# Performance work log

Hardware: AMD Instinct MI355X
Metric: run time of the kernel (lower is better)

The kernel has to match this reference:

```python
import jax, jax.numpy as jnp
import numpy as np

E = 32          # n_routed_experts / num_local_experts
H = 1024        # hidden_size
I = 512         # moe_intermediate_size
G = 8           # n_group
TKG = 4         # topk_group
TOPK = 8        # num_experts_per_tok
NSH = 2         # n_shared_experts
SCALE = 2.5     # routed_scaling_factor


def setup_inputs() -> dict:
    key = jax.random.key(0)
    ks = jax.random.split(key, 10)
    s = 0.02
    return {
        "hidden_states": jax.random.normal(ks[0], (2, 1024, H), jnp.float32),
        # router: linear weight [E, H] and e_score_correction_bias [E]
        "gate_w": jax.random.normal(ks[1], (E, H), jnp.float32) * s,
        "gate_bias": jax.random.normal(ks[2], (E,), jnp.float32) * s,
        # routed experts (stacked SwiGLU weights, torch Linear layout [out, in])
        "w_gate": jax.random.normal(ks[3], (E, I, H), jnp.float32) * s,
        "w_up": jax.random.normal(ks[4], (E, I, H), jnp.float32) * s,
        "w_down": jax.random.normal(ks[5], (E, H, I), jnp.float32) * s,
        # shared experts: one MLP with intermediate = I * NSH
        "sh_gate": jax.random.normal(ks[6], (I * NSH, H), jnp.float32) * s,
        "sh_up": jax.random.normal(ks[7], (I * NSH, H), jnp.float32) * s,
        "sh_down": jax.random.normal(ks[8], (H, I * NSH), jnp.float32) * s,
    }


def reference(hidden_states, gate_w, gate_bias, w_gate, w_up, w_down,
              sh_gate, sh_up, sh_down):
    B, S, Hd = hidden_states.shape
    h = hidden_states.reshape(-1, Hd)                      # [T, H]

    # ---- router (DeepseekV3TopkRouter + route_tokens_to_experts) ----
    logits = h.astype(jnp.float32) @ gate_w.T              # [T, E]
    scores = jax.nn.sigmoid(logits)
    sc = scores + gate_bias                                # scores_for_choice
    # group score = sum of top-2 expert scores within each group
    grp = sc.reshape(-1, G, E // G)                        # [T, G, E/G]
    group_scores = jax.lax.top_k(grp, 2)[0].sum(-1)        # [T, G]
    gidx = jax.lax.top_k(group_scores, TKG)[1]             # [T, TKG]
    gmask = jnp.sum(jax.nn.one_hot(gidx, G, dtype=sc.dtype), axis=1)  # [T, G]
    smask = jnp.repeat(gmask, E // G, axis=1)              # [T, E]
    masked = jnp.where(smask > 0, sc, jnp.zeros_like(sc))  # masked_fill(~mask, 0)
    tki = jax.lax.top_k(masked, TOPK)[1]                   # [T, TOPK]
    tkw = jnp.take_along_axis(scores, tki, axis=1)         # gather raw sigmoid scores
    tkw = tkw / (tkw.sum(-1, keepdims=True) + 1e-20)       # norm_topk_prob
    tkw = tkw * SCALE

    # ---- dispatch-compute-combine (experts_forward) ----
    # combine[t, e] = sum_k tkw[t, k] * [tki[t, k] == e]
    combine = (jax.nn.one_hot(tki, E, dtype=tkw.dtype) * tkw[..., None]).sum(1)  # [T, E]
    g = jax.nn.silu(jnp.einsum('th,eih->tei', h, w_gate))  # [T, E, I]
    u = jnp.einsum('th,eih->tei', h, w_up)                 # [T, E, I]
    routed = jnp.einsum('tei,ehi->th', g * u * combine[:, :, None], w_down)  # [T, H]

    # ---- shared experts ----
    sg = jax.nn.silu(h @ sh_gate.T)
    shared = (sg * (h @ sh_up.T)) @ sh_down.T              # [T, H]

    return (routed + shared).reshape(B, S, Hd)
```

## Files before the change

kernel.cpp:

```cpp
#include <hip/hip_runtime.h>
#include <hip/hip_bf16.h>
#include <cstdint>

#define E_ 32
#define H_ 1024
#define I_ 512
#define G_ 8
#define NSH_ 2
#define SCALE_ 2.5f
#define NROUTED (E_ * I_)
#define PADCAP (16384 + E_ * 128)

typedef unsigned short u16;
using bf16x8_t = __attribute__((ext_vector_type(8))) __bf16;
using f32x4_t  = __attribute__((ext_vector_type(4))) float;

__device__ __forceinline__ u16 f2bf(float x) {
  union { float f; uint32_t u; } v; v.f = x;
  uint32_t u = v.u;
  uint32_t r = (u + 0x7fffu + ((u >> 16) & 1u)) >> 16;
  return (u16)r;
}
__device__ __forceinline__ float bf2f(u16 x) {
  union { uint32_t u; float f; } v; v.u = ((uint32_t)x) << 16; return v.f;
}

__device__ __forceinline__ void load_lds16(const void* g, void* l) {
  __builtin_amdgcn_global_load_lds(
      (const __attribute__((address_space(1))) unsigned int*)g,
      (__attribute__((address_space(3))) unsigned int*)l,
      16, 0, 0);
}

__global__ void cvt_kernel(const float* __restrict__ src, u16* __restrict__ dst, long n4) {
  long i = (long)blockIdx.x * blockDim.x + threadIdx.x;
  if (i >= n4) return;
  float4 v = ((const float4*)src)[i];
  ushort4 o;
  o.x = f2bf(v.x); o.y = f2bf(v.y); o.z = f2bf(v.z); o.w = f2bf(v.w);
  ((ushort4*)dst)[i] = o;
}

#define W4_WG  4194304L
#define W4_WU  8388608L
#define W4_WD  12582912L
#define W4_SHG 12845056L
#define W4_SHU 13107200L
#define W4_TOT 13369344L
__global__ void cvtw_kernel(const float* __restrict__ wg, const float* __restrict__ wu,
                            const float* __restrict__ wd, const float* __restrict__ shg,
                            const float* __restrict__ shu, const float* __restrict__ shd,
                            u16* __restrict__ dst) {
  long i = (long)blockIdx.x * blockDim.x + threadIdx.x;
  long stride = (long)gridDim.x * blockDim.x;
  for (; i < W4_TOT; i += stride) {
    const float* s; long off;
    if (i < W4_WG)       { s = wg;  off = i; }
    else if (i < W4_WU)  { s = wu;  off = i - W4_WG; }
    else if (i < W4_WD)  { s = wd;  off = i - W4_WU; }
    else if (i < W4_SHG) { s = shg; off = i - W4_WD; }
    else if (i < W4_SHU) { s = shu; off = i - W4_SHG; }
    else                 { s = shd; off = i - W4_SHU; }
    float4 v = ((const float4*)s)[off];
    ushort4 o;
    o.x = f2bf(v.x); o.y = f2bf(v.y); o.z = f2bf(v.z); o.w = f2bf(v.w);
    ((ushort4*)dst)[i] = o;
  }
}

__global__ void init_kernel(int* __restrict__ counts, int* __restrict__ cursor,
                            int* __restrict__ tok_list, float* __restrict__ wt_list) {
  int i = blockIdx.x * blockDim.x + threadIdx.x;
  if (i < PADCAP) { tok_list[i] = 0; wt_list[i] = 0.f; }
  if (i < E_) { counts[i] = 0; cursor[i] = 0; }
}

__global__ void gwt_kernel(const float* __restrict__ gw, float* __restrict__ gwT) {
  int i = blockIdx.x * blockDim.x + threadIdx.x;
  if (i >= H_ * E_) return;
  int k = i >> 5, e = i & 31;
  gwT[i] = gw[(long)e * H_ + k];
}

__global__ __launch_bounds__(256) void logits_kernel(
    const float* __restrict__ h, const float* __restrict__ gwT,
    float* __restrict__ logits) {
  __shared__ float sh[8][H_];
  const int tid = threadIdx.x;
  const int t0 = blockIdx.x * 8;
  #pragma unroll
  for (int c = tid; c < 8 * H_ / 4; c += 256) {
    int row = c / (H_ / 4), col = c % (H_ / 4);
    ((float4*)sh[row])[col] = ((const float4*)(h + (size_t)(t0 + row) * H_))[col];
  }
  __syncthreads();
  const int w = tid >> 6, l = tid & 63;
  const int e = l & 31, tl = w * 2 + (l >> 5);
  const float* hp = sh[tl];
  const float* wp = gwT + e;
  float acc = 0.f;
  #pragma unroll 8
  for (int k = 0; k < H_; ++k) acc += hp[k] * wp[(size_t)k * E_];
  logits[(size_t)(t0 + tl) * E_ + e] = acc;
}

__global__ __launch_bounds__(256) void topk_kernel(
    const float* __restrict__ logits, const float* __restrict__ gb,
    int* __restrict__ idx8, float* __restrict__ wt8, int* __restrict__ counts) {
  __shared__ float s_sc[256][33];
  const int lt = threadIdx.x;
  const int t = blockIdx.x * 256 + lt;
  float sc[E_];
  #pragma unroll
  for (int e = 0; e < E_; ++e) {
    float lg = logits[(size_t)t * E_ + e];
    float sig = 1.f / (1.f + __expf(-lg));
    s_sc[lt][e] = sig;
    sc[e] = sig + gb[e];
  }
  float gs[G_];
  #pragma unroll
  for (int g = 0; g < G_; ++g) {
    float a = sc[g * 4], b = sc[g * 4 + 1], c = sc[g * 4 + 2], d = sc[g * 4 + 3];
    float hi1 = fmaxf(a, b), lo1 = fminf(a, b);
    float hi2 = fmaxf(c, d), lo2 = fminf(c, d);
    float m1 = fmaxf(hi1, hi2);
    float m2 = (hi1 >= hi2) ? fmaxf(lo1, hi2) : fmaxf(lo2, hi1);
    gs[g] = m1 + m2;
  }
  unsigned gm = 0;
  #pragma unroll
  for (int r = 0; r < 4; ++r) {
    float bv = -1e30f; int bi = 0;
    #pragma unroll
    for (int g = 0; g < G_; ++g)
      if (!(gm & (1u << g)) && gs[g] > bv) { bv = gs[g]; bi = g; }
    gm |= 1u << bi;
  }
  float msk[E_];
  #pragma unroll
  for (int e = 0; e < E_; ++e)
    msk[e] = ((gm >> (e >> 2)) & 1u) ? sc[e] : 0.f;
  unsigned um = 0; float wsum = 0.f;
  int idxs[8]; float wts[8];
  #pragma unroll
  for (int r = 0; r < 8; ++r) {
    float bv = -1e30f; int bi = 0;
    #pragma unroll
    for (int e = 0; e < E_; ++e)
      if (!(um & (1u << e)) && msk[e] > bv) { bv = msk[e]; bi = e; }
    um |= 1u << bi;
    idxs[r] = bi;
    float wv = s_sc[lt][bi];
    wts[r] = wv; wsum += wv;
  }
  float inv = SCALE_ / (wsum + 1e-20f);
  #pragma unroll
  for (int r = 0; r < 8; ++r) {
    idx8[(size_t)t * 8 + r] = idxs[r];
    wt8[(size_t)t * 8 + r] = wts[r] * inv;
    atomicAdd(&counts[idxs[r]], 1);
  }
}

__global__ void scan_kernel(const int* __restrict__ counts, int* __restrict__ offs) {
  if (threadIdx.x == 0 && blockIdx.x == 0) {
    int run = 0;
    for (int e = 0; e < E_; ++e) {
      offs[e] = run;
      run += ((counts[e] + 127) >> 7) << 7;
    }
    offs[E_] = run;
  }
}

__global__ void fill_kernel(const int* __restrict__ idx8, const float* __restrict__ wt8,
                            const int* __restrict__ offs, int* __restrict__ cursor,
                            int* __restrict__ tok_list, float* __restrict__ wt_list,
                            int* __restrict__ pair_pos, int npair) {
  int i = blockIdx.x * blockDim.x + threadIdx.x;
  if (i >= npair) return;
  int e = idx8[i];
  int p = atomicAdd(&cursor[e], 1);
  int slot = offs[e] + p;
  tok_list[slot] = i >> 3;
  wt_list[slot] = wt8[i];
  pair_pos[i] = slot;
}

__global__ __launch_bounds__(256, 4) void p1_kernel(
    const u16* __restrict__ hbf,
    const u16* __restrict__ bg, const u16* __restrict__ bu,
    const u16* __restrict__ bshg, const u16* __restrict__ bshu,
    const int* __restrict__ counts, const int* __restrict__ offs,
    const int* __restrict__ tok_list, const float* __restrict__ wt_list,
    u16* __restrict__ gu,
    u16* __restrict__ gu_sh,
    int T) {
  const int z = blockIdx.z, tt = blockIdx.y, nb = blockIdx.x;
  const bool sh_e = (z == E_);
  if (!sh_e && nb >= 8) return;
  const int cnt = sh_e ? T : counts[z];
  if (tt * 128 >= cnt) return;
  const int off = sh_e ? 0 : offs[z];

  __shared__ u16 lsA[128 * 64];
  __shared__ u16 lsB0[64 * 64];
  __shared__ u16 lsB1[64 * 64];
  __shared__ int s_tok[128];
  __shared__ float s_wt[128];

  const int tid = threadIdx.x;
  if (tid < 128) {
    if (sh_e) { s_tok[tid] = tt * 128 + tid; s_wt[tid] = 1.0f; }
    else {
      int slot = off + tt * 128 + tid;
      s_tok[tid] = tok_list[slot];
      s_wt[tid] = wt_list[slot];
    }
  }
  __syncthreads();

  const u16* Bg = sh_e ? (bshg + (size_t)(nb * 64) * H_)
                       : (bg + ((size_t)z * I_ + nb * 64) * H_);
  const u16* Bu = sh_e ? (bshu + (size_t)(nb * 64) * H_)
                       : (bu + ((size_t)z * I_ + nb * 64) * H_);

  const int w = tid >> 6, l = tid & 63;
  const int wr = w >> 1, wc = w & 1;
  const int lr = l & 15, lh = l >> 4;
  const int sw = lr & 7;

  f32x4_t acc0[4][2], acc1[4][2];
  #pragma unroll
  for (int m = 0; m < 4; ++m)
    #pragma unroll
    for (int n = 0; n < 2; ++n) {
      acc0[m][n] = (f32x4_t){0.f, 0.f, 0.f, 0.f};
      acc1[m][n] = (f32x4_t){0.f, 0.f, 0.f, 0.f};
    }

  for (int k0 = 0; k0 < H_; k0 += 64) {
    #pragma unroll
    for (int i = 0; i < 4; ++i) {
      int c = tid + 256 * i;
      int row = c >> 3, cb = c & 7;
      int scb = cb ^ (row & 7);
      load_lds16(hbf + (size_t)s_tok[row] * H_ + k0 + scb * 8, (char*)lsA + c * 16);
    }
    #pragma unroll
    for (int i = 0; i < 2; ++i) {
      int c = tid + 256 * i;
      int row = c >> 3, cb = c & 7;
      int scb = cb ^ (row & 7);
      load_lds16(Bg + (size_t)row * H_ + k0 + scb * 8, (char*)lsB0 + c * 16);
      load_lds16(Bu + (size_t)row * H_ + k0 + scb * 8, (char*)lsB1 + c * 16);
    }
    __syncthreads();
    #pragma unroll
    for (int kk = 0; kk < 64; kk += 32) {
      const int sb = kk >> 3;
      const int blk = ((sb + lh) ^ sw) << 3;
      bf16x8_t af[4], b0f[2], b1f[2];
      #pragma unroll
      for (int m = 0; m < 4; ++m)
        af[m] = *(const bf16x8_t*)(lsA + (wr * 64 + m * 16 + lr) * 64 + blk);
      #pragma unroll
      for (int n = 0; n < 2; ++n) {
        b0f[n] = *(const bf16x8_t*)(lsB0 + (wc * 32 + n * 16 + lr) * 64 + blk);
        b1f[n] = *(const bf16x8_t*)(lsB1 + (wc * 32 + n * 16 + lr) * 64 + blk);
      }
      #pragma unroll
      for (int m = 0; m < 4; ++m)
        #pragma unroll
        for (int n = 0; n < 2; ++n) {
          acc0[m][n] = __builtin_amdgcn_mfma_f32_16x16x32_bf16(af[m], b0f[n], acc0[m][n], 0, 0, 0);
          acc1[m][n] = __builtin_amdgcn_mfma_f32_16x16x32_bf16(af[m], b1f[n], acc1[m][n], 0, 0, 0);
        }
    }
    __syncthreads();
  }

  const int ldo = sh_e ? (I_ * NSH_) : I_;
  u16* outp = sh_e ? (gu_sh + (size_t)(tt * 128) * ldo + nb * 64)
                   : (gu + (size_t)(off + tt * 128) * ldo + nb * 64);
  #pragma unroll
  for (int m = 0; m < 4; ++m) {
    #pragma unroll
    for (int n = 0; n < 2; ++n) {
      int col = wc * 32 + n * 16 + lr;
      #pragma unroll
      for (int j = 0; j < 4; ++j) {
        int trow = wr * 64 + m * 16 + lh * 4 + j;
        float gv = acc0[m][n][j], uv = acc1[m][n][j];
        float sv = gv / (1.f + __expf(-gv));
        outp[(size_t)trow * ldo + col] = f2bf(sv * uv * s_wt[trow]);
      }
    }
  }
}

__global__ __launch_bounds__(256, 6) void p2_kernel(
    const u16* __restrict__ gu, const u16* __restrict__ gu_sh,
    const u16* __restrict__ bd,
    const u16* __restrict__ bshd,
    const int* __restrict__ counts, const int* __restrict__ offs,
    u16* __restrict__ part,
    u16* __restrict__ part_sh,
    int T) {
  const int z = blockIdx.z, tt = blockIdx.y, nb = blockIdx.x;
  const bool sh_e = (z == E_);
  const int cnt = sh_e ? T : counts[z];
  if (tt * 128 >= cnt) return;

  __shared__ u16 lsA[128 * 64];
  __shared__ u16 lsB[64 * 64];

  const int tid = threadIdx.x;
  const int w = tid >> 6, l = tid & 63;
  const int wr = w >> 1, wc = w & 1;
  const int lr = l & 15, lh = l >> 4;
  const int sw = lr & 7;

  const int K = sh_e ? (I_ * NSH_) : I_;
  const int NT = K / 64;
  const u16* Ab = sh_e ? (gu_sh + (size_t)(tt * 128) * K)
                       : (gu + (size_t)(offs[z] + tt * 128) * K);
  const u16* Bb = sh_e ? (bshd + (size_t)(nb * 64) * K)
                       : (bd + (size_t)z * H_ * I_ + (size_t)(nb * 64) * K);
  u16* outp = sh_e ? (part_sh + (size_t)(tt * 128) * H_ + nb * 64)
                   : (part + (size_t)(offs[z] + tt * 128) * H_ + nb * 64);

  f32x4_t acc[4][2];
  #pragma unroll
  for (int m = 0; m < 4; ++m)
    #pragma unroll
    for (int n = 0; n < 2; ++n) acc[m][n] = (f32x4_t){0.f, 0.f, 0.f, 0.f};

  for (int s = 0; s < NT; ++s) {
    int k0 = s * 64;
    #pragma unroll
    for (int i = 0; i < 4; ++i) {
      int c = tid + 256 * i;
      int row = c >> 3, cb = c & 7;
      int scb = cb ^ (row & 7);
      load_lds16(Ab + (size_t)row * K + k0 + scb * 8, (char*)lsA + c * 16);
    }
    #pragma unroll
    for (int i = 0; i < 2; ++i) {
      int c = tid + 256 * i;
      int row = c >> 3, cb = c & 7;
      int scb = cb ^ (row & 7);
      load_lds16(Bb + (size_t)row * K + k0 + scb * 8, (char*)lsB + c * 16);
    }
    __syncthreads();
    #pragma unroll
    for (int kk = 0; kk < 64; kk += 32) {
      const int sb = kk >> 3;
      const int blk = ((sb + lh) ^ sw) << 3;
      bf16x8_t af[4], bf[2];
      #pragma unroll
      for (int m = 0; m < 4; ++m)
        af[m] = *(const bf16x8_t*)(lsA + (wr * 64 + m * 16 + lr) * 64 + blk);
      #pragma unroll
      for (int n = 0; n < 2; ++n)
        bf[n] = *(const bf16x8_t*)(lsB + (wc * 32 + n * 16 + lr) * 64 + blk);
      #pragma unroll
      for (int m = 0; m < 4; ++m)
        #pragma unroll
        for (int n = 0; n < 2; ++n)
          acc[m][n] = __builtin_amdgcn_mfma_f32_16x16x32_bf16(af[m], bf[n], acc[m][n], 0, 0, 0);
    }
    __syncthreads();
  }

  #pragma unroll
  for (int m = 0; m < 4; ++m) {
    #pragma unroll
    for (int n = 0; n < 2; ++n) {
      int col = wc * 32 + n * 16 + lr;
      #pragma unroll
      for (int j = 0; j < 4; ++j) {
        int trow = wr * 64 + m * 16 + lh * 4 + j;
        outp[(size_t)trow * H_ + col] = f2bf(acc[m][n][j]);
      }
    }
  }
}

__global__ void combine_kernel(const u16* __restrict__ part, const u16* __restrict__ part_sh,
                               const int* __restrict__ pair_pos, float* __restrict__ out) {
  int t = blockIdx.x;
  int h = threadIdx.x * 4;
  int pp[8];
  #pragma unroll
  for (int s = 0; s < 8; ++s) pp[s] = pair_pos[(long)t * 8 + s];
  ushort4 v = *(const ushort4*)(part_sh + (size_t)t * H_ + h);
  float a0 = bf2f(v.x), a1 = bf2f(v.y), a2 = bf2f(v.z), a3 = bf2f(v.w);
  #pragma unroll
  for (int s = 0; s < 8; ++s) {
    ushort4 u = *(const ushort4*)(part + (size_t)pp[s] * H_ + h);
    a0 += bf2f(u.x); a1 += bf2f(u.y); a2 += bf2f(u.z); a3 += bf2f(u.w);
  }
  float4 o = {a0, a1, a2, a3};
  *(float4*)(out + (size_t)t * H_ + h) = o;
}

extern "C" void kernel_launch(void* const* d_in, const int* in_sizes, int n_in,
                              void* d_out, int out_size, void* d_ws, size_t ws_size,
                              hipStream_t stream) {
  const float* hs  = (const float*)d_in[0];
  const float* gw  = (const float*)d_in[1];
  const float* gb  = (const float*)d_in[2];
  const float* wg  = (const float*)d_in[3];
  const float* wu  = (const float*)d_in[4];
  const float* wd  = (const float*)d_in[5];
  const float* shg = (const float*)d_in[6];
  const float* shu = (const float*)d_in[7];
  const float* shd = (const float*)d_in[8];
  float* out = (float*)d_out;

  const int T = in_sizes[0] / H_;

  char* ws = (char*)d_ws;
  size_t off = 0;
  auto alloc = [&](size_t bytes) {
    char* p = ws + off;
    off += (bytes + 255) & ~(size_t)255;
    return p;
  };
  int*   counts   = (int*)alloc(E_ * 4);
  int*   cursor   = (int*)alloc(E_ * 4);
  int*   offsv    = (int*)alloc((E_ + 1) * 4);
  int*   idx8     = (int*)alloc((size_t)T * 8 * 4);
  float* wt8      = (float*)alloc((size_t)T * 8 * 4);
  int*   pair_pos = (int*)alloc((size_t)T * 8 * 4);
  int*   tok_list = (int*)alloc(PADCAP * 4);
  float* wt_list  = (float*)alloc(PADCAP * 4);
  float* gwT      = (float*)alloc((size_t)H_ * E_ * 4);
  float* logits   = (float*)alloc((size_t)T * E_ * 4);
  u16* hbf     = (u16*)alloc((size_t)T * H_ * 2);
  u16* wbf     = (u16*)alloc((size_t)W4_TOT * 4 * 2);
  u16* gu      = (u16*)alloc((size_t)PADCAP * I_ * 2);
  u16* gu_sh   = (u16*)alloc((size_t)T * I_ * NSH_ * 2);
  u16* part    = (u16*)alloc((size_t)PADCAP * H_ * 2);
  u16* part_sh = (u16*)alloc((size_t)T * H_ * 2);
  if (off > ws_size) return;

  u16* bg   = wbf;
  u16* bu   = wbf + (size_t)NROUTED * H_;
  u16* bd   = bu + (size_t)NROUTED * H_;
  u16* bshg = bd + (size_t)E_ * H_ * I_;
  u16* bshu = bshg + (size_t)I_ * NSH_ * H_;
  u16* bshd = bshu + (size_t)I_ * NSH_ * H_;

  hipLaunchKernelGGL(init_kernel, dim3((PADCAP + 255) / 256), dim3(256), 0, stream,
                     counts, cursor, tok_list, wt_list);

  hipLaunchKernelGGL(gwt_kernel, dim3((H_ * E_ + 255) / 256), dim3(256), 0, stream, gw, gwT);
  hipLaunchKernelGGL(logits_kernel, dim3(T / 8), dim3(256), 0, stream, hs, gwT, logits);
  hipLaunchKernelGGL(topk_kernel, dim3(T / 256), dim3(256), 0, stream,
                     logits, gb, idx8, wt8, counts);
  hipLaunchKernelGGL(scan_kernel, dim3(1), dim3(64), 0, stream, counts, offsv);
  hipLaunchKernelGGL(fill_kernel, dim3((T * 8 + 255) / 256), dim3(256), 0, stream,
                     idx8, wt8, offsv, cursor, tok_list, wt_list, pair_pos, T * 8);

  {
    long n4 = (long)T * H_ / 4;
    hipLaunchKernelGGL(cvt_kernel, dim3((int)((n4 + 255) / 256)), dim3(256), 0, stream,
                       hs, hbf, n4);
  }
  hipLaunchKernelGGL(cvtw_kernel, dim3(2048), dim3(256), 0, stream,
                     wg, wu, wd, shg, shu, shd, wbf);

  hipLaunchKernelGGL(p1_kernel, dim3(16, T / 128, E_ + 1), dim3(256), 0, stream,
                     hbf, bg, bu, bshg, bshu, counts, offsv, tok_list, wt_list,
                     gu, gu_sh, T);

  hipLaunchKernelGGL(p2_kernel, dim3(16, T / 128, E_ + 1), dim3(256), 0, stream,
                     gu, gu_sh, bd, bshd, counts, offsv, part, part_sh, T);

  hipLaunchKernelGGL(combine_kernel, dim3(T), dim3(256), 0, stream,
                     part, part_sh, pair_pos, out);
}
```

Before: 312.4 us.

## Persistent atomic tile queues for expert GEMMs and fuse small prep kernels

```diff
diff --git a/kernel.cpp b/kernel.cpp
--- a/kernel.cpp
+++ b/kernel.cpp
@@ -32,66 +32,59 @@
       16, 0, 0);
 }
 
-__global__ void cvt_kernel(const float* __restrict__ src, u16* __restrict__ dst, long n4) {
-  long i = (long)blockIdx.x * blockDim.x + threadIdx.x;
-  if (i >= n4) return;
-  float4 v = ((const float4*)src)[i];
-  ushort4 o;
-  o.x = f2bf(v.x); o.y = f2bf(v.y); o.z = f2bf(v.z); o.w = f2bf(v.w);
-  ((ushort4*)dst)[i] = o;
-}
-
-#define W4_WG  4194304L
-#define W4_WU  8388608L
-#define W4_WD  12582912L
-#define W4_SHG 12845056L
-#define W4_SHU 13107200L
-#define W4_TOT 13369344L
+#define OFF_BU   16777216L
+#define OFF_BD   33554432L
+#define OFF_BSHG 50331648L
+#define OFF_BSHU 51380224L
+#define OFF_BSHD 52428800L
+#define WBF_TOT  53477376L
+
+__global__ void init_kernel(const float* __restrict__ gw, float* __restrict__ gwT,
+                            int* __restrict__ counts, int* __restrict__ cursor,
+                            int* __restrict__ qheads,
+                            int* __restrict__ tok_list, float* __restrict__ wt_list) {
+  int i = blockIdx.x * blockDim.x + threadIdx.x;
+  if (i < H_ * E_) {
+    int k = i >> 5, e = i & 31;
+    gwT[i] = gw[(long)e * H_ + k];
+  }
+  if (i < PADCAP) { tok_list[i] = 0; wt_list[i] = 0.f; }
+  if (i < E_) { counts[i] = 0; cursor[i] = 0; }
+  if (i < 2) qheads[i] = 0;
+}
+
 __global__ void cvtw_kernel(const float* __restrict__ wg, const float* __restrict__ wu,
-                            const float* __restrict__ wd, const float* __restrict__ shg,
-                            const float* __restrict__ shu, const float* __restrict__ shd,
-                            u16* __restrict__ dst) {
+                            const float* __restrict__ shg, const float* __restrict__ shu,
+                            u16* __restrict__ wbf) {
   long i = (long)blockIdx.x * blockDim.x + threadIdx.x;
   long stride = (long)gridDim.x * blockDim.x;
-  for (; i < W4_TOT; i += stride) {
-    const float* s; long off;
-    if (i < W4_WG)       { s = wg;  off = i; }
-    else if (i < W4_WU)  { s = wu;  off = i - W4_WG; }
-    else if (i < W4_WD)  { s = wd;  off = i - W4_WU; }
-    else if (i < W4_SHG) { s = shg; off = i - W4_WD; }
-    else if (i < W4_SHU) { s = shu; off = i - W4_SHG; }
-    else                 { s = shd; off = i - W4_SHU; }
+  for (; i < 8912896L; i += stride) {
+    const float* s; long off; long dofs;
+    if (i < 4194304L)      { s = wg;  off = i;            dofs = i * 4; }
+    else if (i < 8388608L) { s = wu;  off = i - 4194304L; dofs = OFF_BU + off * 4; }
+    else if (i < 8650752L) { s = shg; off = i - 8388608L; dofs = OFF_BSHG + off * 4; }
+    else                   { s = shu; off = i - 8650752L; dofs = OFF_BSHU + off * 4; }
     float4 v = ((const float4*)s)[off];
     ushort4 o;
     o.x = f2bf(v.x); o.y = f2bf(v.y); o.z = f2bf(v.z); o.w = f2bf(v.w);
-    ((ushort4*)dst)[i] = o;
-  }
-}
-
-__global__ void init_kernel(int* __restrict__ counts, int* __restrict__ cursor,
-                            int* __restrict__ tok_list, float* __restrict__ wt_list) {
-  int i = blockIdx.x * blockDim.x + threadIdx.x;
-  if (i < PADCAP) { tok_list[i] = 0; wt_list[i] = 0.f; }
-  if (i < E_) { counts[i] = 0; cursor[i] = 0; }
-}
-
-__global__ void gwt_kernel(const float* __restrict__ gw, float* __restrict__ gwT) {
-  int i = blockIdx.x * blockDim.x + threadIdx.x;
-  if (i >= H_ * E_) return;
-  int k = i >> 5, e = i & 31;
-  gwT[i] = gw[(long)e * H_ + k];
+    *(ushort4*)(wbf + dofs) = o;
+  }
 }
 
 __global__ __launch_bounds__(256) void logits_kernel(
     const float* __restrict__ h, const float* __restrict__ gwT,
-    float* __restrict__ logits) {
+    float* __restrict__ logits, u16* __restrict__ hbf) {
   __shared__ float sh[8][H_];
   const int tid = threadIdx.x;
   const int t0 = blockIdx.x * 8;
   #pragma unroll
   for (int c = tid; c < 8 * H_ / 4; c += 256) {
     int row = c / (H_ / 4), col = c % (H_ / 4);
-    ((float4*)sh[row])[col] = ((const float4*)(h + (size_t)(t0 + row) * H_))[col];
+    float4 v = ((const float4*)(h + (size_t)(t0 + row) * H_))[col];
+    ((float4*)sh[row])[col] = v;
+    ushort4 o;
+    o.x = f2bf(v.x); o.y = f2bf(v.y); o.z = f2bf(v.z); o.w = f2bf(v.w);
+    ((ushort4*)(hbf + (size_t)(t0 + row) * H_))[col] = o;
   }
   __syncthreads();
   const int w = tid >> 6, l = tid & 63;
@@ -163,26 +156,20 @@
   }
 }
 
-__global__ void scan_kernel(const int* __restrict__ counts, int* __restrict__ offs) {
-  if (threadIdx.x == 0 && blockIdx.x == 0) {
-    int run = 0;
-    for (int e = 0; e < E_; ++e) {
-      offs[e] = run;
-      run += ((counts[e] + 127) >> 7) << 7;
-    }
-    offs[E_] = run;
-  }
-}
-
 __global__ void fill_kernel(const int* __restrict__ idx8, const float* __restrict__ wt8,
-                            const int* __restrict__ offs, int* __restrict__ cursor,
+                            const int* __restrict__ counts, int* __restrict__ cursor,
                             int* __restrict__ tok_list, float* __restrict__ wt_list,
                             int* __restrict__ pair_pos, int npair) {
   int i = blockIdx.x * blockDim.x + threadIdx.x;
   if (i >= npair) return;
   int e = idx8[i];
+  int offz = 0;
+  for (int k = 0; k < E_; ++k) {
+    if (k == e) break;
+    offz += ((counts[k] + 127) >> 7) << 7;
+  }
   int p = atomicAdd(&cursor[e], 1);
-  int slot = offs[e] + p;
+  int slot = offz + p;
   tok_list[slot] = i >> 3;
   wt_list[slot] = wt8[i];
   pair_pos[i] = slot;
@@ -190,199 +177,260 @@
 
 __global__ __launch_bounds__(256, 4) void p1_kernel(
     const u16* __restrict__ hbf,
-    const u16* __restrict__ bg, const u16* __restrict__ bu,
-    const u16* __restrict__ bshg, const u16* __restrict__ bshu,
-    const int* __restrict__ counts, const int* __restrict__ offs,
+    const u16* __restrict__ wbf,
+    const int* __restrict__ counts,
     const int* __restrict__ tok_list, const float* __restrict__ wt_list,
+    int* __restrict__ qheads,
+    const float* __restrict__ wd, const float* __restrict__ shd,
+    u16* __restrict__ wbf_mut,
     u16* __restrict__ gu,
     u16* __restrict__ gu_sh,
     int T) {
-  const int z = blockIdx.z, tt = blockIdx.y, nb = blockIdx.x;
-  const bool sh_e = (z == E_);
-  if (!sh_e && nb >= 8) return;
-  const int cnt = sh_e ? T : counts[z];
-  if (tt * 128 >= cnt) return;
-  const int off = sh_e ? 0 : offs[z];
-
   __shared__ u16 lsA[128 * 64];
   __shared__ u16 lsB0[64 * 64];
   __shared__ u16 lsB1[64 * 64];
   __shared__ int s_tok[128];
   __shared__ float s_wt[128];
+  __shared__ int s_cnt[E_], s_off[E_], s_ntt[E_];
+  __shared__ int s_tot, s_tile;
 
   const int tid = threadIdx.x;
-  if (tid < 128) {
-    if (sh_e) { s_tok[tid] = tt * 128 + tid; s_wt[tid] = 1.0f; }
-    else {
-      int slot = off + tt * 128 + tid;
-      s_tok[tid] = tok_list[slot];
-      s_wt[tid] = wt_list[slot];
-    }
-  }
+  if (tid < E_) s_cnt[tid] = counts[tid];
   __syncthreads();
-
-  const u16* Bg = sh_e ? (bshg + (size_t)(nb * 64) * H_)
-                       : (bg + ((size_t)z * I_ + nb * 64) * H_);
-  const u16* Bu = sh_e ? (bshu + (size_t)(nb * 64) * H_)
-                       : (bu + ((size_t)z * I_ + nb * 64) * H_);
+  if (tid == 0) {
+    int run = 0, tot = 0;
+    for (int e = 0; e < E_; ++e) {
+      s_off[e] = run;
+      int nt = (s_cnt[e] + 127) >> 7;
+      s_ntt[e] = nt;
+      run += nt << 7;
+      tot += nt * 8;
+    }
+    s_tot = tot + (T / 128) * 16;
+  }
 
   const int w = tid >> 6, l = tid & 63;
   const int wr = w >> 1, wc = w & 1;
   const int lr = l & 15, lh = l >> 4;
   const int sw = lr & 7;
 
-  f32x4_t acc0[4][2], acc1[4][2];
-  #pragma unroll
-  for (int m = 0; m < 4; ++m)
+  for (;;) {
+    __syncthreads();
+    if (tid == 0) s_tile = atomicAdd(&qheads[0], 1);
+    __syncthreads();
+    int q = s_tile;
+    if (q >= s_tot) break;
+
+    int z = 0, rem = q;
+    for (; z < E_; ++z) { int t = s_ntt[z] * 8; if (rem < t) break; rem -= t; }
+    const bool sh_e = (z == E_);
+    int tt, nb;
+    if (sh_e) { tt = rem >> 4; nb = rem & 15; }
+    else      { tt = rem >> 3; nb = rem & 7; }
+    const int off = sh_e ? 0 : s_off[z];
+
+    if (tid < 128) {
+      if (sh_e) { s_tok[tid] = tt * 128 + tid; s_wt[tid] = 1.0f; }
+      else {
+        int slot = off + tt * 128 + tid;
+        s_tok[tid] = tok_list[slot];
+        s_wt[tid] = wt_list[slot];
+      }
+    }
+    __syncthreads();
+
+    const u16* Bg = sh_e ? (wbf + OFF_BSHG + (size_t)(nb * 64) * H_)
+                         : (wbf + ((size_t)z * I_ + nb * 64) * H_);
+    const u16* Bu = sh_e ? (wbf + OFF_BSHU + (size_t)(nb * 64) * H_)
+                         : (wbf + OFF_BU + ((size_t)z * I_ + nb * 64) * H_);
+
+    f32x4_t acc0[4][2], acc1[4][2];
     #pragma unroll
-    for (int n = 0; n < 2; ++n) {
-      acc0[m][n] = (f32x4_t){0.f, 0.f, 0.f, 0.f};
-      acc1[m][n] = (f32x4_t){0.f, 0.f, 0.f, 0.f};
-    }
-
-  for (int k0 = 0; k0 < H_; k0 += 64) {
+    for (int m = 0; m < 4; ++m)
+      #pragma unroll
+      for (int n = 0; n < 2; ++n) {
+        acc0[m][n] = (f32x4_t){0.f, 0.f, 0.f, 0.f};
+        acc1[m][n] = (f32x4_t){0.f, 0.f, 0.f, 0.f};
+      }
+
+    for (int k0 = 0; k0 < H_; k0 += 64) {
+      #pragma unroll
+      for (int i = 0; i < 4; ++i) {
+        int c = tid + 256 * i;
+        int row = c >> 3, cb = c & 7;
+        int scb = cb ^ (row & 7);
+        load_lds16(hbf + (size_t)s_tok[row] * H_ + k0 + scb * 8, (char*)lsA + c * 16);
+      }
+      #pragma unroll
+      for (int i = 0; i < 2; ++i) {
+        int c = tid + 256 * i;
+        int row = c >> 3, cb = c & 7;
+        int scb = cb ^ (row & 7);
+        load_lds16(Bg + (size_t)row * H_ + k0 + scb * 8, (char*)lsB0 + c * 16);
+        load_lds16(Bu + (size_t)row * H_ + k0 + scb * 8, (char*)lsB1 + c * 16);
+      }
+      __syncthreads();
+      #pragma unroll
+      for (int kk = 0; kk < 64; kk += 32) {
+        const int sb = kk >> 3;
+        const int blk = ((sb + lh) ^ sw) << 3;
+        bf16x8_t af[4], b0f[2], b1f[2];
+        #pragma unroll
+        for (int m = 0; m < 4; ++m)
+          af[m] = *(const bf16x8_t*)(lsA + (wr * 64 + m * 16 + lr) * 64 + blk);
+        #pragma unroll
+        for (int n = 0; n < 2; ++n) {
+          b0f[n] = *(const bf16x8_t*)(lsB0 + (wc * 32 + n * 16 + lr) * 64 + blk);
+          b1f[n] = *(const bf16x8_t*)(lsB1 + (wc * 32 + n * 16 + lr) * 64 + blk);
+        }
+        #pragma unroll
+        for (int m = 0; m < 4; ++m)
+          #pragma unroll
+          for (int n = 0; n < 2; ++n) {
+            acc0[m][n] = __builtin_amdgcn_mfma_f32_16x16x32_bf16(af[m], b0f[n], acc0[m][n], 0, 0, 0);
+            acc1[m][n] = __builtin_amdgcn_mfma_f32_16x16x32_bf16(af[m], b1f[n], acc1[m][n], 0, 0, 0);
+          }
+      }
+      __syncthreads();
+    }
+
+    const int ldo = sh_e ? (I_ * NSH_) : I_;
+    u16* outp = sh_e ? (gu_sh + (size_t)(tt * 128) * ldo + nb * 64)
+                     : (gu + (size_t)(off + tt * 128) * ldo + nb * 64);
     #pragma unroll
-    for (int i = 0; i < 4; ++i) {
-      int c = tid + 256 * i;
-      int row = c >> 3, cb = c & 7;
-      int scb = cb ^ (row & 7);
-      load_lds16(hbf + (size_t)s_tok[row] * H_ + k0 + scb * 8, (char*)lsA + c * 16);
-    }
-    #pragma unroll
-    for (int i = 0; i < 2; ++i) {
-      int c = tid + 256 * i;
-      int row = c >> 3, cb = c & 7;
-      int scb = cb ^ (row & 7);
-      load_lds16(Bg + (size_t)row * H_ + k0 + scb * 8, (char*)lsB0 + c * 16);
-      load_lds16(Bu + (size_t)row * H_ + k0 + scb * 8, (char*)lsB1 + c * 16);
-    }
-    __syncthreads();
-    #pragma unroll
-    for (int kk = 0; kk < 64; kk += 32) {
-      const int sb = kk >> 3;
-      const int blk = ((sb + lh) ^ sw) << 3;
-      bf16x8_t af[4], b0f[2], b1f[2];
-      #pragma unroll
-      for (int m = 0; m < 4; ++m)
-        af[m] = *(const bf16x8_t*)(lsA + (wr * 64 + m * 16 + lr) * 64 + blk);
+    for (int m = 0; m < 4; ++m) {
       #pragma unroll
       for (int n = 0; n < 2; ++n) {
-        b0f[n] = *(const bf16x8_t*)(lsB0 + (wc * 32 + n * 16 + lr) * 64 + blk);
-        b1f[n] = *(const bf16x8_t*)(lsB1 + (wc * 32 + n * 16 + lr) * 64 + blk);
-      }
-      #pragma unroll
-      for (int m = 0; m < 4; ++m)
-        #pragma unroll
-        for (int n = 0; n < 2; ++n) {
-          acc0[m][n] = __builtin_amdgcn_mfma_f32_16x16x32_bf16(af[m], b0f[n], acc0[m][n], 0, 0, 0);
-          acc1[m][n] = __builtin_amdgcn_mfma_f32_16x16x32_bf16(af[m], b1f[n], acc1[m][n], 0, 0, 0);
+        int col = wc * 32 + n * 16 + lr;
+        #pragma unroll
+        for (int j = 0; j < 4; ++j) {
+          int trow = wr * 64 + m * 16 + lh * 4 + j;
+          float gv = acc0[m][n][j], uv = acc1[m][n][j];
+          float sv = gv / (1.f + __expf(-gv));
+          outp[(size_t)trow * ldo + col] = f2bf(sv * uv * s_wt[trow]);
         }
-    }
-    __syncthreads();
-  }
-
-  const int ldo = sh_e ? (I_ * NSH_) : I_;
-  u16* outp = sh_e ? (gu_sh + (size_t)(tt * 128) * ldo + nb * 64)
-                   : (gu + (size_t)(off + tt * 128) * ldo + nb * 64);
-  #pragma unroll
-  for (int m = 0; m < 4; ++m) {
-    #pragma unroll
-    for (int n = 0; n < 2; ++n) {
-      int col = wc * 32 + n * 16 + lr;
-      #pragma unroll
-      for (int j = 0; j < 4; ++j) {
-        int trow = wr * 64 + m * 16 + lh * 4 + j;
-        float gv = acc0[m][n][j], uv = acc1[m][n][j];
-        float sv = gv / (1.f + __expf(-gv));
-        outp[(size_t)trow * ldo + col] = f2bf(sv * uv * s_wt[trow]);
-      }
-    }
+      }
+    }
+  }
+
+  const long WD4 = 4194304L, TOT4 = 4456448L;
+  for (long i = (long)blockIdx.x * 256 + tid; i < TOT4; i += (long)gridDim.x * 256) {
+    float4 v; long dofs;
+    if (i < WD4) { v = ((const float4*)wd)[i]; dofs = OFF_BD + i * 4; }
+    else { v = ((const float4*)shd)[i - WD4]; dofs = OFF_BSHD + (i - WD4) * 4; }
+    ushort4 o;
+    o.x = f2bf(v.x); o.y = f2bf(v.y); o.z = f2bf(v.z); o.w = f2bf(v.w);
+    *(ushort4*)(wbf_mut + dofs) = o;
   }
 }
 
 __global__ __launch_bounds__(256, 6) void p2_kernel(
     const u16* __restrict__ gu, const u16* __restrict__ gu_sh,
-    const u16* __restrict__ bd,
-    const u16* __restrict__ bshd,
-    const int* __restrict__ counts, const int* __restrict__ offs,
+    const u16* __restrict__ wbf,
+    const int* __restrict__ counts,
+    int* __restrict__ qheads,
     u16* __restrict__ part,
     u16* __restrict__ part_sh,
     int T) {
-  const int z = blockIdx.z, tt = blockIdx.y, nb = blockIdx.x;
-  const bool sh_e = (z == E_);
-  const int cnt = sh_e ? T : counts[z];
-  if (tt * 128 >= cnt) return;
-
   __shared__ u16 lsA[128 * 64];
   __shared__ u16 lsB[64 * 64];
+  __shared__ int s_cnt[E_], s_off[E_], s_ntt[E_];
+  __shared__ int s_tot, s_tile;
 
   const int tid = threadIdx.x;
+  if (tid < E_) s_cnt[tid] = counts[tid];
+  __syncthreads();
+  if (tid == 0) {
+    int run = 0, tot = 0;
+    for (int e = 0; e < E_; ++e) {
+      s_off[e] = run;
+      int nt = (s_cnt[e] + 127) >> 7;
+      s_ntt[e] = nt;
+      run += nt << 7;
+      tot += nt * 16;
+    }
+    s_tot = tot + (T / 128) * 16;
+  }
+
   const int w = tid >> 6, l = tid & 63;
   const int wr = w >> 1, wc = w & 1;
   const int lr = l & 15, lh = l >> 4;
   const int sw = lr & 7;
 
-  const int K = sh_e ? (I_ * NSH_) : I_;
-  const int NT = K / 64;
-  const u16* Ab = sh_e ? (gu_sh + (size_t)(tt * 128) * K)
-                       : (gu + (size_t)(offs[z] + tt * 128) * K);
-  const u16* Bb = sh_e ? (bshd + (size_t)(nb * 64) * K)
-                       : (bd + (size_t)z * H_ * I_ + (size_t)(nb * 64) * K);
-  u16* outp = sh_e ? (part_sh + (size_t)(tt * 128) * H_ + nb * 64)
-                   : (part + (size_t)(offs[z] + tt * 128) * H_ + nb * 64);
-
-  f32x4_t acc[4][2];
-  #pragma unroll
-  for (int m = 0; m < 4; ++m)
+  for (;;) {
+    __syncthreads();
+    if (tid == 0) s_tile = atomicAdd(&qheads[1], 1);
+    __syncthreads();
+    int q = s_tile;
+    if (q >= s_tot) break;
+
+    int z = 0, rem = q;
+    for (; z < E_; ++z) { int t = s_ntt[z] * 16; if (rem < t) break; rem -= t; }
+    const bool sh_e = (z == E_);
+    int tt = rem >> 4, nb = rem & 15;
+
+    const int K = sh_e ? (I_ * NSH_) : I_;
+    const int NT = K / 64;
+    const u16* Ab = sh_e ? (gu_sh + (size_t)(tt * 128) * K)
+                         : (gu + (size_t)(s_off[z] + tt * 128) * K);
+    const u16* Bb = sh_e ? (wbf + OFF_BSHD + (size_t)(nb * 64) * K)
+                         : (wbf + OFF_BD + (size_t)z * H_ * I_ + (size_t)(nb * 64) * K);
+    u16* outp = sh_e ? (part_sh + (size_t)(tt * 128) * H_ + nb * 64)
+                     : (part + (size_t)(s_off[z] + tt * 128) * H_ + nb * 64);
+
+    f32x4_t acc[4][2];
     #pragma unroll
-    for (int n = 0; n < 2; ++n) acc[m][n] = (f32x4_t){0.f, 0.f, 0.f, 0.f};
-
-  for (int s = 0; s < NT; ++s) {
-    int k0 = s * 64;
+    for (int m = 0; m < 4; ++m)
+      #pragma unroll
+      for (int n = 0; n < 2; ++n) acc[m][n] = (f32x4_t){0.f, 0.f, 0.f, 0.f};
+
+    for (int s = 0; s < NT; ++s) {
+      int k0 = s * 64;
+      #pragma unroll
+      for (int i = 0; i < 4; ++i) {
+        int c = tid + 256 * i;
+        int row = c >> 3, cb = c & 7;
+        int scb = cb ^ (row & 7);
+        load_lds16(Ab + (size_t)row * K + k0 + scb * 8, (char*)lsA + c * 16);
+      }
+      #pragma unroll
+      for (int i = 0; i < 2; ++i) {
+        int c = tid + 256 * i;
+        int row = c >> 3, cb = c & 7;
+        int scb = cb ^ (row & 7);
+        load_lds16(Bb + (size_t)row * K + k0 + scb * 8, (char*)lsB + c * 16);
+      }
+      __syncthreads();
+      #pragma unroll
+      for (int kk = 0; kk < 64; kk += 32) {
+        const int sb = kk >> 3;
+        const int blk = ((sb + lh) ^ sw) << 3;
+        bf16x8_t af[4], bf[2];
+        #pragma unroll
+        for (int m = 0; m < 4; ++m)
+          af[m] = *(const bf16x8_t*)(lsA + (wr * 64 + m * 16 + lr) * 64 + blk);
+        #pragma unroll
+        for (int n = 0; n < 2; ++n)
+          bf[n] = *(const bf16x8_t*)(lsB + (wc * 32 + n * 16 + lr) * 64 + blk);
+        #pragma unroll
+        for (int m = 0; m < 4; ++m)
+          #pragma unroll
+          for (int n = 0; n < 2; ++n)
+            acc[m][n] = __builtin_amdgcn_mfma_f32_16x16x32_bf16(af[m], bf[n], acc[m][n], 0, 0, 0);
+      }
+      __syncthreads();
+    }
+
     #pragma unroll
-    for (int i = 0; i < 4; ++i) {
-      int c = tid + 256 * i;
-      int row = c >> 3, cb = c & 7;
-      int scb = cb ^ (row & 7);
-      load_lds16(Ab + (size_t)row * K + k0 + scb * 8, (char*)lsA + c * 16);
-    }
-    #pragma unroll
-    for (int i = 0; i < 2; ++i) {
-      int c = tid + 256 * i;
-      int row = c >> 3, cb = c & 7;
-      int scb = cb ^ (row & 7);
-      load_lds16(Bb + (size_t)row * K + k0 + scb * 8, (char*)lsB + c * 16);
-    }
-    __syncthreads();
-    #pragma unroll
-    for (int kk = 0; kk < 64; kk += 32) {
-      const int sb = kk >> 3;
-      const int blk = ((sb + lh) ^ sw) << 3;
-      bf16x8_t af[4], bf[2];
-      #pragma unroll
-      for (int m = 0; m < 4; ++m)
-        af[m] = *(const bf16x8_t*)(lsA + (wr * 64 + m * 16 + lr) * 64 + blk);
-      #pragma unroll
-      for (int n = 0; n < 2; ++n)
-        bf[n] = *(const bf16x8_t*)(lsB + (wc * 32 + n * 16 + lr) * 64 + blk);
-      #pragma unroll
-      for (int m = 0; m < 4; ++m)
-        #pragma unroll
-        for (int n = 0; n < 2; ++n)
-          acc[m][n] = __builtin_amdgcn_mfma_f32_16x16x32_bf16(af[m], bf[n], acc[m][n], 0, 0, 0);
-    }
-    __syncthreads();
-  }
-
-  #pragma unroll
-  for (int m = 0; m < 4; ++m) {
-    #pragma unroll
-    for (int n = 0; n < 2; ++n) {
-      int col = wc * 32 + n * 16 + lr;
-      #pragma unroll
-      for (int j = 0; j < 4; ++j) {
-        int trow = wr * 64 + m * 16 + lh * 4 + j;
-        outp[(size_t)trow * H_ + col] = f2bf(acc[m][n][j]);
+    for (int m = 0; m < 4; ++m) {
+      #pragma unroll
+      for (int n = 0; n < 2; ++n) {
+        int col = wc * 32 + n * 16 + lr;
+        #pragma unroll
+        for (int j = 0; j < 4; ++j) {
+          int trow = wr * 64 + m * 16 + lh * 4 + j;
+          outp[(size_t)trow * H_ + col] = f2bf(acc[m][n][j]);
+        }
       }
     }
   }
@@ -431,7 +479,7 @@
   };
   int*   counts   = (int*)alloc(E_ * 4);
   int*   cursor   = (int*)alloc(E_ * 4);
-  int*   offsv    = (int*)alloc((E_ + 1) * 4);
+  int*   qheads   = (int*)alloc(2 * 4);
   int*   idx8     = (int*)alloc((size_t)T * 8 * 4);
   float* wt8      = (float*)alloc((size_t)T * 8 * 4);
   int*   pair_pos = (int*)alloc((size_t)T * 8 * 4);
@@ -440,45 +488,32 @@
   float* gwT      = (float*)alloc((size_t)H_ * E_ * 4);
   float* logits   = (float*)alloc((size_t)T * E_ * 4);
   u16* hbf     = (u16*)alloc((size_t)T * H_ * 2);
-  u16* wbf     = (u16*)alloc((size_t)W4_TOT * 4 * 2);
+  u16* wbf     = (u16*)alloc((size_t)WBF_TOT * 2);
   u16* gu      = (u16*)alloc((size_t)PADCAP * I_ * 2);
   u16* gu_sh   = (u16*)alloc((size_t)T * I_ * NSH_ * 2);
   u16* part    = (u16*)alloc((size_t)PADCAP * H_ * 2);
   u16* part_sh = (u16*)alloc((size_t)T * H_ * 2);
   if (off > ws_size) return;
 
-  u16* bg   = wbf;
-  u16* bu   = wbf + (size_t)NROUTED * H_;
-  u16* bd   = bu + (size_t)NROUTED * H_;
-  u16* bshg = bd + (size_t)E_ * H_ * I_;
-  u16* bshu = bshg + (size_t)I_ * NSH_ * H_;
-  u16* bshd = bshu + (size_t)I_ * NSH_ * H_;
-
-  hipLaunchKernelGGL(init_kernel, dim3((PADCAP + 255) / 256), dim3(256), 0, stream,
-                     counts, cursor, tok_list, wt_list);
-
-  hipLaunchKernelGGL(gwt_kernel, dim3((H_ * E_ + 255) / 256), dim3(256), 0, stream, gw, gwT);
-  hipLaunchKernelGGL(logits_kernel, dim3(T / 8), dim3(256), 0, stream, hs, gwT, logits);
+  hipLaunchKernelGGL(init_kernel, dim3(128), dim3(256), 0, stream,
+                     gw, gwT, counts, cursor, qheads, tok_list, wt_list);
+
+  hipLaunchKernelGGL(logits_kernel, dim3(T / 8), dim3(256), 0, stream,
+                     hs, gwT, logits, hbf);
   hipLaunchKernelGGL(topk_kernel, dim3(T / 256), dim3(256), 0, stream,
                      logits, gb, idx8, wt8, counts);
-  hipLaunchKernelGGL(scan_kernel, dim3(1), dim3(64), 0, stream, counts, offsv);
   hipLaunchKernelGGL(fill_kernel, dim3((T * 8 + 255) / 256), dim3(256), 0, stream,
-                     idx8, wt8, offsv, cursor, tok_list, wt_list, pair_pos, T * 8);
-
-  {
-    long n4 = (long)T * H_ / 4;
-    hipLaunchKernelGGL(cvt_kernel, dim3((int)((n4 + 255) / 256)), dim3(256), 0, stream,
-                       hs, hbf, n4);
-  }
-  hipLaunchKernelGGL(cvtw_kernel, dim3(2048), dim3(256), 0, stream,
-                     wg, wu, wd, shg, shu, shd, wbf);
-
-  hipLaunchKernelGGL(p1_kernel, dim3(16, T / 128, E_ + 1), dim3(256), 0, stream,
-                     hbf, bg, bu, bshg, bshu, counts, offsv, tok_list, wt_list,
-                     gu, gu_sh, T);
-
-  hipLaunchKernelGGL(p2_kernel, dim3(16, T / 128, E_ + 1), dim3(256), 0, stream,
-                     gu, gu_sh, bd, bshd, counts, offsv, part, part_sh, T);
+                     idx8, wt8, counts, cursor, tok_list, wt_list, pair_pos, T * 8);
+
+  hipLaunchKernelGGL(cvtw_kernel, dim3(4096), dim3(256), 0, stream,
+                     wg, wu, shg, shu, wbf);
+
+  hipLaunchKernelGGL(p1_kernel, dim3(1024), dim3(256), 0, stream,
+                     hbf, wbf, counts, tok_list, wt_list, qheads,
+                     wd, shd, wbf, gu, gu_sh, T);
+
+  hipLaunchKernelGGL(p2_kernel, dim3(1536), dim3(256), 0, stream,
+                     gu, gu_sh, wbf, counts, qheads, part, part_sh, T);
 
   hipLaunchKernelGGL(combine_kernel, dim3(T), dim3(256), 0, stream,
                      part, part_sh, pair_pos, out);
```

Measured after the change: 360.6 us. 15.4% more time.
